# Kernel optimization log

Hardware: AMD Instinct MI355X
Metric: run time of the kernel (lower is better)

## Reference

```python
import jax, jax.numpy as jnp
import numpy as np
from jax.scipy.special import logsumexp


def setup_inputs() -> dict:
    key = jax.random.key(0)
    k = jax.random.split(key, 8)
    B, T, K, L = 32, 128, 16, 16
    s = 0.05
    y_batch = jax.random.uniform(k[0], (B, T, 1, 28, 28), dtype=jnp.float32)
    enc_w1 = jax.random.normal(k[1], (400, 784), dtype=jnp.float32) * s
    enc_b1 = jnp.zeros((400,), jnp.float32)
    enc_w2 = jax.random.normal(k[2], (2 * L, 400), dtype=jnp.float32) * s
    enc_b2 = jnp.zeros((2 * L,), jnp.float32)
    dec_fc_w = jax.random.normal(k[3], (400, L + K), dtype=jnp.float32) * s
    dec_fc_b = jnp.zeros((400,), jnp.float32)
    dec_w = jax.random.normal(k[4], (784, 400), dtype=jnp.float32) * s
    dec_b = jnp.zeros((784,), jnp.float32)
    log_pi = jnp.zeros((K,), jnp.float32)
    log_A = jax.random.normal(k[5], (K, K), dtype=jnp.float32)
    log_A = log_A.at[jnp.arange(K), jnp.arange(K)].set(-1e9)  # fill_diagonal_(-1e9)
    eps = jax.random.normal(k[6], (B * T, L), dtype=jnp.float32)
    return dict(y_batch=y_batch, enc_w1=enc_w1, enc_b1=enc_b1, enc_w2=enc_w2,
                enc_b2=enc_b2, dec_fc_w=dec_fc_w, dec_fc_b=dec_fc_b, dec_w=dec_w,
                dec_b=dec_b, log_pi=log_pi, log_A=log_A, eps=eps)


def reference(y_batch, enc_w1, enc_b1, enc_w2, enc_b2, dec_fc_w, dec_fc_b,
              dec_w, dec_b, log_pi, log_A, eps):
    B, T = y_batch.shape[0], y_batch.shape[1]
    K = log_pi.shape[0]
    L = eps.shape[1]
    N = B * T
    # ---- VAE emission log-likelihoods (compute_log_bk); dropout in eval mode ----
    y_flat = y_batch.reshape(N, 784)
    h = jax.nn.relu(y_flat @ enc_w1.T + enc_b1)                 # [N,400]
    ml = h @ enc_w2.T + enc_b2                                   # [N,2L]
    mu, logvar = ml[:, :L], ml[:, L:]
    z = mu + eps * jnp.exp(0.5 * logvar)                         # reparameterize
    # decode(z, one_hot(k)) for all k at once: split cat-linear into z part + k column
    Wz, Wx = dec_fc_w[:, :L], dec_fc_w[:, L:]                    # [400,L],[400,K]
    base = z @ Wz.T + dec_fc_b                                   # [N,400]
    hk = jax.nn.relu(base[None, :, :] + Wx.T[:, None, :])        # [K,N,400]
    y_rec = jax.nn.sigmoid(jnp.einsum('knh,oh->kno', hk, dec_w) + dec_b)  # [K,N,784]
    # binary_cross_entropy with torch's log clamp at -100
    logp = jnp.clip(jnp.log(y_rec), -100.0, None)
    log1mp = jnp.clip(jnp.log(1.0 - y_rec), -100.0, None)
    bce = -(y_flat[None] * logp + (1.0 - y_flat[None]) * log1mp)  # [K,N,784]
    recon = bce.sum(-1) / 100.0                                   # [K,N]
    log_bk = (-recon).reshape(K, B, T).transpose(1, 2, 0)         # [B,T,K]
    # ---- forward-backward in log domain ----
    lp = jnp.log(jax.nn.softmax(log_pi) + 1e-9)
    lA = jnp.log(jax.nn.softmax(log_A, axis=1) + 1e-9)
    lb_rest = jnp.moveaxis(log_bk[:, 1:], 1, 0)                   # [T-1,B,K]
    a0 = lp + log_bk[:, 0]                                        # [B,K]

    def fstep(prev, lb_t):
        cur = logsumexp(prev[:, :, None] + lA[None], axis=1) + lb_t
        return cur, cur

    _, alphas = jax.lax.scan(fstep, a0, lb_rest)
    log_alpha = jnp.concatenate([a0[:, None], jnp.moveaxis(alphas, 0, 1)], axis=1)  # [B,T,K]

    bT = jnp.zeros((B, K), log_bk.dtype)

    def bstep(nxt, lb_t1):
        cur = logsumexp(lA[None] + (lb_t1 + nxt)[:, None, :], axis=2)
        return cur, cur

    _, betas = jax.lax.scan(bstep, bT, lb_rest, reverse=True)     # betas[t] = beta_t, t=0..T-2
    log_beta = jnp.concatenate([jnp.moveaxis(betas, 0, 1), bT[:, None]], axis=1)  # [B,T,K]

    lg = log_alpha + log_beta
    log_gamma = lg - logsumexp(lg, axis=2, keepdims=True)

    lxi = (log_alpha[:, :-1, :, None] + lA[None, None]
           + (log_bk[:, 1:] + log_beta[:, 1:])[:, :, None, :])    # [B,T-1,K,K]
    lxi = lxi - logsumexp(lxi, axis=(2, 3), keepdims=True)
    return jnp.exp(log_gamma), jnp.exp(lxi)
```

## Files before the change

kernel.cpp:

```cpp
#include <hip/hip_runtime.h>
#include <math.h>


typedef _Float16 h8v __attribute__((ext_vector_type(8)));
typedef _Float16 h4v __attribute__((ext_vector_type(4)));
typedef float f16v __attribute__((ext_vector_type(16)));

__global__ __launch_bounds__(256)
void k_prep(const float* __restrict__ dw, const float* __restrict__ ew1,
            _Float16* __restrict__ dwh, _Float16* __restrict__ w1h,
            float* __restrict__ lb) {
  int idx = blockIdx.x * 256 + threadIdx.x;
  if (idx < 65536) lb[idx] = 0.f;
  if (idx < 896 * 448) {
    int o = idx / 448, h2 = idx - o * 448;
    float v = (o < 784 && h2 < 400) ? dw[o * 400 + h2] : 0.f;
    dwh[idx] = (_Float16)v;
  } else if (idx < 896 * 448 + 512 * 800) {
    int j = idx - 896 * 448;
    int i = j / 800, kc = j - i * 800;
    float v = (i < 400 && kc < 784) ? ew1[i * 784 + kc] : 0.f;
    w1h[j] = (_Float16)v;
  }
}

#define E1ST 40
__global__ __launch_bounds__(256, 2)
void k_enc1(const float* __restrict__ y, const _Float16* __restrict__ w1h,
            const float* __restrict__ b1, float* __restrict__ hout) {
  __shared__ __align__(16) _Float16 Ah[64 * E1ST];
  __shared__ __align__(16) _Float16 Bh[128 * E1ST];
  const int tid = threadIdx.x;
  const int i0 = blockIdx.x * 128;
  const int n0 = blockIdx.y * 64;
  const int wav = tid >> 6, lane = tid & 63;
  const int wn = wav >> 1, wi = wav & 1;
  const int ln = lane & 31, kg = lane >> 5;

  f16v acc[2];
#pragma unroll
  for (int j = 0; j < 2; ++j)
#pragma unroll
    for (int r = 0; r < 16; ++r) acc[j][r] = 0.f;

  const int ar = tid >> 3, ac4 = (tid & 7) * 4;
  const int br = tid >> 2, bg = (tid & 3) * 8;

#pragma unroll 1
  for (int hc = 0; hc < 25; ++hc) {
    const int h0 = hc * 32;
    __syncthreads();
#pragma unroll
    for (int it = 0; it < 2; ++it) {
      int r = ar + 32 * it;
      float4 a = make_float4(0.f, 0.f, 0.f, 0.f);
      if (h0 + ac4 < 784) a = *(const float4*)&y[(n0 + r) * 784 + h0 + ac4];
      h4v hv;
      hv[0] = (_Float16)a.x; hv[1] = (_Float16)a.y;
      hv[2] = (_Float16)a.z; hv[3] = (_Float16)a.w;
      *(h4v*)&Ah[r * E1ST + ac4] = hv;
    }
#pragma unroll
    for (int it = 0; it < 2; ++it) {
      int r = br + 64 * it;
      *(h8v*)&Bh[r * E1ST + bg] = *(const h8v*)&w1h[(i0 + r) * 800 + h0 + bg];
    }
    __syncthreads();
#pragma unroll
    for (int kk = 0; kk < 2; ++kk) {
      const int ko = kk * 16 + kg * 8;
      h8v a  = *(const h8v*)&Ah[(wn * 32 + ln) * E1ST + ko];
      h8v b0 = *(const h8v*)&Bh[(wi * 64 + ln) * E1ST + ko];
      h8v b1 = *(const h8v*)&Bh[(wi * 64 + 32 + ln) * E1ST + ko];
      acc[0] = __builtin_amdgcn_mfma_f32_32x32x16_f16(a, b0, acc[0], 0, 0, 0);
      acc[1] = __builtin_amdgcn_mfma_f32_32x32x16_f16(a, b1, acc[1], 0, 0, 0);
    }
  }
#pragma unroll
  for (int j = 0; j < 2; ++j) {
    const int i = i0 + wi * 64 + j * 32 + ln;
    if (i < 400) {
      const float bias = b1[i];
#pragma unroll
      for (int reg = 0; reg < 16; ++reg) {
        const int row = n0 + wn * 32 + (reg & 3) + 8 * (reg >> 2) + 4 * kg;
        hout[row * 400 + i] = fmaxf(acc[j][reg] + bias, 0.f);
      }
    }
  }
}

__global__ __launch_bounds__(128, 4)
void k_enc2z(const float* __restrict__ h, const float* __restrict__ w2,
             const float* __restrict__ b2, const float* __restrict__ eps,
             float* __restrict__ z) {
  __shared__ __align__(16) float h_lds[4 * 400];
  __shared__ __align__(16) float w2_lds[32 * 404];
  __shared__ float ml_lds[4 * 32];
  const int tid = threadIdx.x;
  const int n0 = blockIdx.x * 4;
  for (int idx = tid; idx < 400; idx += 128) {
    int r = idx / 100, c = idx % 100;
    *(float4*)&h_lds[r * 400 + c * 4] = *(const float4*)&h[(n0 + r) * 400 + c * 4];
  }
  for (int idx = tid; idx < 3200; idx += 128) {
    int r = idx / 100, c = idx % 100;
    *(float4*)&w2_lds[r * 404 + c * 4] = *(const float4*)&w2[r * 400 + c * 4];
  }
  __syncthreads();
  const int c_ = tid & 31, n_ = tid >> 5;
  float acc = 0.f;
  for (int q = 0; q < 100; ++q) {
    float4 hv = *(const float4*)&h_lds[n_ * 400 + q * 4];
    float4 wv = *(const float4*)&w2_lds[c_ * 404 + q * 4];
    acc += hv.x * wv.x + hv.y * wv.y + hv.z * wv.z + hv.w * wv.w;
  }
  ml_lds[n_ * 32 + c_] = acc + b2[c_];
  __syncthreads();
  if (tid < 64) {
    int n2 = tid >> 4, l = tid & 15;
    float mu = ml_lds[n2 * 32 + l];
    float lv = ml_lds[n2 * 32 + 16 + l];
    z[(n0 + n2) * 16 + l] = mu + eps[(n0 + n2) * 16 + l] * expf(0.5f * lv);
  }
}

__global__ __launch_bounds__(256, 4)
void k_base(const float* __restrict__ z, const float* __restrict__ dfw,
            const float* __restrict__ dfb, float* __restrict__ basep) {
  __shared__ float z_lds[16 * 16];
  __shared__ __align__(16) float wz_lds[400 * 20];
  const int tid = threadIdx.x;
  const int n0 = blockIdx.x * 16;
  if (tid < 64) {
    int n = tid >> 2, c = (tid & 3) * 4;
    *(float4*)&z_lds[n * 16 + c] = *(const float4*)&z[(n0 + n) * 16 + c];
  }
  for (int idx = tid; idx < 1600; idx += 256) {
    int i = idx >> 2, c = (idx & 3) * 4;
    *(float4*)&wz_lds[i * 20 + c] = *(const float4*)&dfw[i * 32 + c];
  }
  __syncthreads();
  for (int idx = tid; idx < 7168; idx += 256) {
    int n = idx / 448, i = idx - n * 448;
    float acc = 0.f;
    if (i < 400) {
      acc = dfb[i];
#pragma unroll
      for (int q = 0; q < 4; ++q) {
        float4 zv = *(const float4*)&z_lds[n * 16 + q * 4];
        float4 wv = *(const float4*)&wz_lds[i * 20 + q * 4];
        acc += zv.x * wv.x + zv.y * wv.y + zv.z * wv.z + zv.w * wv.w;
      }
    }
    basep[(n0 + n) * 448 + i] = acc;
  }
}

#define DST 72
__global__ __launch_bounds__(256, 2)
void k_dec(const float* __restrict__ basep, const float* __restrict__ dfw,
           const _Float16* __restrict__ dwh, const float* __restrict__ decb,
           const float* __restrict__ y, float* __restrict__ lb) {
  __shared__ __align__(16) _Float16 Ah[128 * DST];
  __shared__ __align__(16) _Float16 Bh[128 * DST];
  __shared__ float wx[448];
  __shared__ float red[256];

  const int tid = threadIdx.x;
  const int id  = blockIdx.x;
  const int lin = (id & 7) * 448 + (id >> 3);
  const int n_i = lin / 112;
  const int rem = lin - n_i * 112;
  const int k   = rem / 7;
  const int ot  = rem - k * 7;
  const int n0  = n_i * 128;
  const int o0  = ot * 128;
  const bool full = (ot < 6);

  const int wav = tid >> 6, lane = tid & 63;
  const int wn = wav >> 1, wo = wav & 1;
  const int ln = lane & 31, kg = lane >> 5;

  for (int i = tid; i < 448; i += 256) wx[i] = (i < 400) ? dfw[i * 32 + 16 + k] : 0.f;

  const int ar = tid >> 4, ac4 = (tid & 15) * 4;
  const int br = tid >> 3, bg = (tid & 7) * 8;
  const float* aptr = basep + (long)(n0 + ar) * 448 + ac4;

  float4 apf[8];
#pragma unroll
  for (int it = 0; it < 8; ++it) apf[it] = *(const float4*)&aptr[(16 * it) * 448];

  f16v acc[2][2];
#pragma unroll
  for (int i = 0; i < 2; ++i)
#pragma unroll
    for (int j = 0; j < 2; ++j)
#pragma unroll
      for (int r = 0; r < 16; ++r) acc[i][j][r] = 0.f;

#pragma unroll 1
  for (int hc = 0; hc < 7; ++hc) {
    const int h0 = hc * 64;
    h8v bpf[4];
#pragma unroll
    for (int it = 0; it < 4; ++it)
      bpf[it] = *(const h8v*)&dwh[(o0 + br + 32 * it) * 448 + h0 + bg];
    __syncthreads();
    {
      float4 w = *(const float4*)&wx[h0 + ac4];
#pragma unroll
      for (int it = 0; it < 8; ++it) {
        int r = ar + 16 * it;
        h4v hv;
        hv[0] = (_Float16)fmaxf(apf[it].x + w.x, 0.f);
        hv[1] = (_Float16)fmaxf(apf[it].y + w.y, 0.f);
        hv[2] = (_Float16)fmaxf(apf[it].z + w.z, 0.f);
        hv[3] = (_Float16)fmaxf(apf[it].w + w.w, 0.f);
        *(h4v*)&Ah[r * DST + ac4] = hv;
      }
    }
#pragma unroll
    for (int it = 0; it < 4; ++it)
      *(h8v*)&Bh[(br + 32 * it) * DST + bg] = bpf[it];
    __syncthreads();
    if (hc < 6) {
      const int hn = (hc + 1) * 64;
#pragma unroll
      for (int it = 0; it < 8; ++it)
        apf[it] = *(const float4*)&aptr[(16 * it) * 448 + hn];
    }
#pragma unroll
    for (int kk = 0; kk < 4; ++kk) {
      const int ko = kk * 16 + kg * 8;
      h8v a0 = *(const h8v*)&Ah[(wn * 64 + ln) * DST + ko];
      h8v a1 = *(const h8v*)&Ah[(wn * 64 + 32 + ln) * DST + ko];
      h8v b0 = *(const h8v*)&Bh[(wo * 64 + ln) * DST + ko];
      h8v b1 = *(const h8v*)&Bh[(wo * 64 + 32 + ln) * DST + ko];
      if (full) {
        acc[0][0] = __builtin_amdgcn_mfma_f32_32x32x16_f16(a0, b0, acc[0][0], 0, 0, 0);
        acc[1][0] = __builtin_amdgcn_mfma_f32_32x32x16_f16(a1, b0, acc[1][0], 0, 0, 0);
        acc[0][1] = __builtin_amdgcn_mfma_f32_32x32x16_f16(a0, b1, acc[0][1], 0, 0, 0);
        acc[1][1] = __builtin_amdgcn_mfma_f32_32x32x16_f16(a1, b1, acc[1][1], 0, 0, 0);
      } else if (wo == 0) {
        acc[0][0] = __builtin_amdgcn_mfma_f32_32x32x16_f16(a0, b0, acc[0][0], 0, 0, 0);
        acc[1][0] = __builtin_amdgcn_mfma_f32_32x32x16_f16(a1, b0, acc[1][0], 0, 0, 0);
      }
    }
  }
  const int obase = o0 + wo * 64;
  const float bj0 = (obase + ln < 784) ? decb[obase + ln] : 0.f;
  const float bj1 = (obase + 32 + ln < 784) ? decb[obase + 32 + ln] : 0.f;
#pragma unroll
  for (int i = 0; i < 2; ++i) {
#pragma unroll
    for (int reg = 0; reg < 16; ++reg) {
      const int row = wn * 64 + i * 32 + (reg & 3) + 8 * (reg >> 2) + 4 * kg;
      float v = 0.f;
#pragma unroll
      for (int j = 0; j < 2; ++j) {
        const int o = obase + j * 32 + ln;
        if (o < 784) {
          float x = acc[i][j][reg] + (j ? bj1 : bj0);
          float yv = y[(n0 + row) * 784 + o];
          float spx = fmaxf(x, 0.f) + __logf(1.f + __expf(-fabsf(x)));
          float t2 = fminf(spx, 100.f);
          float t1 = fminf(spx - x, 100.f);
          v += t2 + yv * (t1 - t2);
        }
      }
      v += __shfl_xor(v, 1, 64);
      v += __shfl_xor(v, 2, 64);
      v += __shfl_xor(v, 4, 64);
      v += __shfl_xor(v, 8, 64);
      v += __shfl_xor(v, 16, 64);
      if (ln == 0) red[wo * 128 + row] = v;
    }
  }
  __syncthreads();
  if (tid < 128) {
    float s = red[tid] + red[128 + tid];
    atomicAdd(&lb[(n0 + tid) * 16 + k], s);
  }
}

__global__ __launch_bounds__(256, 2)
void k_hmm(const float* __restrict__ lb, const float* __restrict__ lpi,
           const float* __restrict__ lA, float* __restrict__ out,
           float* __restrict__ g_ah, float* __restrict__ g_pb,
           float* __restrict__ g_sinv, float* __restrict__ g_Al) {
  __shared__ float btl[128 * 16];
  __shared__ float ah[128 * 16];
  __shared__ float bh[128 * 16];
  __shared__ float braw[128 * 16];
  __shared__ float A_l[16 * 17];
  __shared__ float pi_l[16];
  const int tid = threadIdx.x;
  const int b = blockIdx.x;

  for (int idx = tid; idx < 512; idx += 256) {
    float4 v = *(const float4*)&lb[b * 2048 + idx * 4];
    v.x *= -0.01f; v.y *= -0.01f; v.z *= -0.01f; v.w *= -0.01f;
    *(float4*)&btl[idx * 4] = v;
  }
  if (tid < 16) {
    const int j = tid;
    float m = -1e30f;
#pragma unroll
    for (int q = 0; q < 16; ++q) m = fmaxf(m, lA[j * 16 + q]);
    float e[16]; float s = 0.f;
#pragma unroll
    for (int q = 0; q < 16; ++q) { e[q] = expf(lA[j * 16 + q] - m); s += e[q]; }
    float inv = 1.f / s;
#pragma unroll
    for (int q = 0; q < 16; ++q) {
      float v = e[q] * inv + 1e-9f;
      A_l[j * 17 + q] = v;
      g_Al[j * 16 + q] = v;
    }
  } else if (tid == 16) {
    float m = -1e30f;
#pragma unroll
    for (int q = 0; q < 16; ++q) m = fmaxf(m, lpi[q]);
    float e[16]; float s = 0.f;
#pragma unroll
    for (int q = 0; q < 16; ++q) { e[q] = expf(lpi[q] - m); s += e[q]; }
    float inv = 1.f / s;
#pragma unroll
    for (int q = 0; q < 16; ++q) pi_l[q] = e[q] * inv + 1e-9f;
  }
  __syncthreads();
  if (tid < 128) {
    const int t = tid;
    float v[16]; float m = -1e30f;
#pragma unroll
    for (int q = 0; q < 16; ++q) { v[q] = btl[t * 16 + q]; m = fmaxf(m, v[q]); }
#pragma unroll
    for (int q = 0; q < 16; ++q) btl[t * 16 + q] = expf(v[q] - m);
  }
  __syncthreads();
  const int lane = tid & 63;
  const int kk = lane & 15, grp = lane >> 4;
  if (tid < 64) {
    float v0 = pi_l[kk] * btl[kk];
    float ss0 = v0;
    ss0 += __shfl_xor(ss0, 1, 64); ss0 += __shfl_xor(ss0, 2, 64);
    ss0 += __shfl_xor(ss0, 4, 64); ss0 += __shfl_xor(ss0, 8, 64);
    if (grp == 0) ah[kk] = v0 / ss0;
    for (int t = 1; t < 128; ++t) {
      float acc = 0.f;
#pragma unroll
      for (int jj = 0; jj < 4; ++jj) {
        int j = grp * 4 + jj;
        acc = fmaf(ah[(t - 1) * 16 + j], A_l[j * 17 + kk], acc);
      }
      acc += __shfl_xor(acc, 16, 64);
      acc += __shfl_xor(acc, 32, 64);
      float v = acc * btl[t * 16 + kk];
      float ss = v;
      ss += __shfl_xor(ss, 1, 64); ss += __shfl_xor(ss, 2, 64);
      ss += __shfl_xor(ss, 4, 64); ss += __shfl_xor(ss, 8, 64);
      if (grp == 0) ah[t * 16 + kk] = v / ss;
    }
  } else if (tid < 128) {
    if (grp == 0) bh[127 * 16 + kk] = 1.f;
    for (int t = 126; t >= 0; --t) {
      float acc = 0.f;
#pragma unroll
      for (int q = 0; q < 4; ++q) {
        int k2 = grp * 4 + q;
        acc = fmaf(A_l[kk * 17 + k2], btl[(t + 1) * 16 + k2] * bh[(t + 1) * 16 + k2], acc);
      }
      acc += __shfl_xor(acc, 16, 64);
      acc += __shfl_xor(acc, 32, 64);
      float ss = acc;
      ss += __shfl_xor(ss, 1, 64); ss += __shfl_xor(ss, 2, 64);
      ss += __shfl_xor(ss, 4, 64); ss += __shfl_xor(ss, 8, 64);
      if (grp == 0) { braw[t * 16 + kk] = acc; bh[t * 16 + kk] = acc / ss; }
    }
  }
  __syncthreads();
  if (tid < 128) {
    const int t = tid;
    float g[16]; float s2 = 0.f;
#pragma unroll
    for (int q = 0; q < 16; ++q) { g[q] = ah[t * 16 + q] * bh[t * 16 + q]; s2 += g[q]; }
    float inv = 1.f / s2;
#pragma unroll
    for (int c = 0; c < 4; ++c) {
      float4 o;
      o.x = g[c * 4 + 0] * inv; o.y = g[c * 4 + 1] * inv;
      o.z = g[c * 4 + 2] * inv; o.w = g[c * 4 + 3] * inv;
      *(float4*)&out[(b * 128 + t) * 16 + c * 4] = o;
      float4 av = *(float4*)&ah[t * 16 + c * 4];
      *(float4*)&g_ah[(b * 128 + t) * 16 + c * 4] = av;
      float4 p;
      p.x = btl[t * 16 + c * 4 + 0] * bh[t * 16 + c * 4 + 0];
      p.y = btl[t * 16 + c * 4 + 1] * bh[t * 16 + c * 4 + 1];
      p.z = btl[t * 16 + c * 4 + 2] * bh[t * 16 + c * 4 + 2];
      p.w = btl[t * 16 + c * 4 + 3] * bh[t * 16 + c * 4 + 3];
      *(float4*)&g_pb[(b * 128 + t) * 16 + c * 4] = p;
    }
  } else {
    const int t = tid - 128;
    if (t < 127) {
      float s2 = 0.f;
#pragma unroll
      for (int q = 0; q < 16; ++q) s2 += ah[t * 16 + q] * braw[t * 16 + q];
      g_sinv[b * 128 + t] = 1.f / s2;
    }
  }
}

__global__ __launch_bounds__(256)
void k_xi(const float* __restrict__ g_ah, const float* __restrict__ g_pb,
          const float* __restrict__ g_sinv, const float* __restrict__ g_Al,
          float* __restrict__ out) {
  const int b = blockIdx.x, t = blockIdx.y;
  const int tid = threadIdx.x;
  const int j = tid >> 4, k2 = tid & 15;
  float val = g_ah[(b * 128 + t) * 16 + j] * g_Al[j * 16 + k2] *
              g_pb[(b * 128 + t + 1) * 16 + k2] * g_sinv[b * 128 + t];
  out[65536 + (b * 127 + t) * 256 + tid] = val;
}

extern "C" void kernel_launch(void* const* d_in, const int* in_sizes, int n_in,
                              void* d_out, int out_size, void* d_ws, size_t ws_size,
                              hipStream_t stream) {
  (void)in_sizes; (void)n_in; (void)out_size; (void)ws_size;
  const float* y   = (const float*)d_in[0];
  const float* ew1 = (const float*)d_in[1];
  const float* eb1 = (const float*)d_in[2];
  const float* ew2 = (const float*)d_in[3];
  const float* eb2 = (const float*)d_in[4];
  const float* dfw = (const float*)d_in[5];
  const float* dfb = (const float*)d_in[6];
  const float* dw  = (const float*)d_in[7];
  const float* db  = (const float*)d_in[8];
  const float* lpi = (const float*)d_in[9];
  const float* lA  = (const float*)d_in[10];
  const float* eps = (const float*)d_in[11];
  float* out = (float*)d_out;

  float* ws = (float*)d_ws;
  float* h      = ws;
  float* basep  = ws;
  float* z      = ws + 1835008;
  float* lb     = z + 65536;
  _Float16* dwh = (_Float16*)(lb + 65536);
  _Float16* w1h = dwh + 896 * 448;
  float* g_ah   = (float*)(w1h + 512 * 800);
  float* g_pb   = g_ah + 65536;
  float* g_sinv = g_pb + 65536;
  float* g_Al   = g_sinv + 4096;

  k_prep<<<3168, 256, 0, stream>>>(dw, ew1, dwh, w1h, lb);
  k_enc1<<<dim3(4, 64), 256, 0, stream>>>(y, w1h, eb1, h);
  k_enc2z<<<1024, 128, 0, stream>>>(h, ew2, eb2, eps, z);
  k_base<<<256, 256, 0, stream>>>(z, dfw, dfb, basep);
  k_dec<<<3584, 256, 0, stream>>>(basep, dfw, dwh, db, y, lb);
  k_hmm<<<32, 256, 0, stream>>>(lb, lpi, lA, out, g_ah, g_pb, g_sinv, g_Al);
  k_xi<<<dim3(32, 127), 256, 0, stream>>>(g_ah, g_pb, g_sinv, g_Al, out);
}
```

Baseline: 347.6 us.

## Precompute fp16 hidden activations per state and stream into decoder via global_load_lds

Adds a kernel that builds relu(base + Wx[k]) for all 16 states as an fp16 tensor in workspace. A new decoder GEMM then loads A and B tiles straight into LDS with global_load_lds, using XOR swizzling instead of padded rows. This removes the per-tile in-kernel construction and conversion of hidden activations, at the cost of writing and re-reading a roughly 59 MB fp16 buffer. The new path only runs when the workspace is large enough. Separately, the encoder second layer now handles 16 rows per block with 4 accumulators per thread, so each W2 load is reused four times.

```diff
diff --git a/kernel.cpp b/kernel.cpp
--- a/kernel.cpp
+++ b/kernel.cpp
@@ -5,6 +5,12 @@
 typedef _Float16 h8v __attribute__((ext_vector_type(8)));
 typedef _Float16 h4v __attribute__((ext_vector_type(4)));
 typedef float f16v __attribute__((ext_vector_type(16)));
+
+__device__ __forceinline__ void gll16(const void* g, void* l) {
+  __builtin_amdgcn_global_load_lds(
+      (const __attribute__((address_space(1))) void*)g,
+      (__attribute__((address_space(3))) void*)l, 16, 0, 0);
+}
 
 __global__ __launch_bounds__(256)
 void k_prep(const float* __restrict__ dw, const float* __restrict__ ew1,
@@ -90,35 +96,45 @@
   }
 }
 
-__global__ __launch_bounds__(128, 4)
+__global__ __launch_bounds__(128, 2)
 void k_enc2z(const float* __restrict__ h, const float* __restrict__ w2,
              const float* __restrict__ b2, const float* __restrict__ eps,
              float* __restrict__ z) {
-  __shared__ __align__(16) float h_lds[4 * 400];
+  __shared__ __align__(16) float h_lds[16 * 400];
   __shared__ __align__(16) float w2_lds[32 * 404];
-  __shared__ float ml_lds[4 * 32];
-  const int tid = threadIdx.x;
-  const int n0 = blockIdx.x * 4;
-  for (int idx = tid; idx < 400; idx += 128) {
-    int r = idx / 100, c = idx % 100;
+  __shared__ float ml_lds[16 * 32];
+  const int tid = threadIdx.x;
+  const int n0 = blockIdx.x * 16;
+  for (int idx = tid; idx < 1600; idx += 128) {
+    int r = idx / 100, c = idx - r * 100;
     *(float4*)&h_lds[r * 400 + c * 4] = *(const float4*)&h[(n0 + r) * 400 + c * 4];
   }
   for (int idx = tid; idx < 3200; idx += 128) {
-    int r = idx / 100, c = idx % 100;
+    int r = idx / 100, c = idx - r * 100;
     *(float4*)&w2_lds[r * 404 + c * 4] = *(const float4*)&w2[r * 400 + c * 4];
   }
   __syncthreads();
-  const int c_ = tid & 31, n_ = tid >> 5;
-  float acc = 0.f;
+  const int c_ = tid & 31, n4 = tid >> 5;
+  float a0 = 0.f, a1 = 0.f, a2 = 0.f, a3 = 0.f;
   for (int q = 0; q < 100; ++q) {
-    float4 hv = *(const float4*)&h_lds[n_ * 400 + q * 4];
     float4 wv = *(const float4*)&w2_lds[c_ * 404 + q * 4];
-    acc += hv.x * wv.x + hv.y * wv.y + hv.z * wv.z + hv.w * wv.w;
-  }
-  ml_lds[n_ * 32 + c_] = acc + b2[c_];
-  __syncthreads();
-  if (tid < 64) {
-    int n2 = tid >> 4, l = tid & 15;
+    float4 h0 = *(const float4*)&h_lds[(n4 * 4 + 0) * 400 + q * 4];
+    float4 h1 = *(const float4*)&h_lds[(n4 * 4 + 1) * 400 + q * 4];
+    float4 h2 = *(const float4*)&h_lds[(n4 * 4 + 2) * 400 + q * 4];
+    float4 h3 = *(const float4*)&h_lds[(n4 * 4 + 3) * 400 + q * 4];
+    a0 += h0.x * wv.x + h0.y * wv.y + h0.z * wv.z + h0.w * wv.w;
+    a1 += h1.x * wv.x + h1.y * wv.y + h1.z * wv.z + h1.w * wv.w;
+    a2 += h2.x * wv.x + h2.y * wv.y + h2.z * wv.z + h2.w * wv.w;
+    a3 += h3.x * wv.x + h3.y * wv.y + h3.z * wv.z + h3.w * wv.w;
+  }
+  const float bb = b2[c_];
+  ml_lds[(n4 * 4 + 0) * 32 + c_] = a0 + bb;
+  ml_lds[(n4 * 4 + 1) * 32 + c_] = a1 + bb;
+  ml_lds[(n4 * 4 + 2) * 32 + c_] = a2 + bb;
+  ml_lds[(n4 * 4 + 3) * 32 + c_] = a3 + bb;
+  __syncthreads();
+  for (int t = tid; t < 256; t += 128) {
+    int n2 = t >> 4, l = t & 15;
     float mu = ml_lds[n2 * 32 + l];
     float lv = ml_lds[n2 * 32 + 16 + l];
     z[(n0 + n2) * 16 + l] = mu + eps[(n0 + n2) * 16 + l] * expf(0.5f * lv);
@@ -157,11 +173,152 @@
   }
 }
 
+__global__ __launch_bounds__(256, 4)
+void k_hk(const float* __restrict__ basep, const float* __restrict__ dfw,
+          _Float16* __restrict__ hkh) {
+  __shared__ float wxT[16 * 448];
+  const int tid = threadIdx.x;
+  const int n0 = blockIdx.x * 8;
+  for (int idx = tid; idx < 7168; idx += 256) {
+    int k = idx / 448, hh = idx - k * 448;
+    wxT[idx] = (hh < 400) ? dfw[hh * 32 + 16 + k] : 0.f;
+  }
+  __syncthreads();
+  for (int s = tid; s < 448; s += 256) {
+    int r = s / 56, c8 = s - r * 56;
+    const float* bp = &basep[(size_t)(n0 + r) * 448 + c8 * 8];
+    float4 b0 = *(const float4*)bp;
+    float4 b1 = *(const float4*)(bp + 4);
+#pragma unroll
+    for (int k = 0; k < 16; ++k) {
+      const float* wp = &wxT[k * 448 + c8 * 8];
+      float4 w0 = *(const float4*)wp;
+      float4 w1 = *(const float4*)(wp + 4);
+      h8v o;
+      o[0] = (_Float16)fmaxf(b0.x + w0.x, 0.f);
+      o[1] = (_Float16)fmaxf(b0.y + w0.y, 0.f);
+      o[2] = (_Float16)fmaxf(b0.z + w0.z, 0.f);
+      o[3] = (_Float16)fmaxf(b0.w + w0.w, 0.f);
+      o[4] = (_Float16)fmaxf(b1.x + w1.x, 0.f);
+      o[5] = (_Float16)fmaxf(b1.y + w1.y, 0.f);
+      o[6] = (_Float16)fmaxf(b1.z + w1.z, 0.f);
+      o[7] = (_Float16)fmaxf(b1.w + w1.w, 0.f);
+      *(h8v*)&hkh[((size_t)k * 4096 + n0 + r) * 448 + c8 * 8] = o;
+    }
+  }
+}
+
+__global__ __launch_bounds__(256, 2)
+void k_dec2(const _Float16* __restrict__ hkh, const _Float16* __restrict__ dwh,
+            const float* __restrict__ decb, const float* __restrict__ y,
+            float* __restrict__ lb) {
+  __shared__ __align__(16) _Float16 Ah[128 * 64];
+  __shared__ __align__(16) _Float16 Bh[128 * 64];
+  __shared__ float red[256];
+
+  const int tid = threadIdx.x;
+  const int id  = blockIdx.x;
+  const int lin = (id & 7) * 448 + (id >> 3);
+  const int n_i = lin / 112;
+  const int rem = lin - n_i * 112;
+  const int k   = rem / 7;
+  const int ot  = rem - k * 7;
+  const int n0  = n_i * 128;
+  const int o0  = ot * 128;
+
+  const int wav = tid >> 6, lane = tid & 63;
+  const int wn = wav >> 1, wo = wav & 1;
+  const int ln = lane & 31, kg = lane >> 5;
+
+  const int l8 = lane >> 3, l7 = lane & 7;
+  const int swh = (l7 * 8) ^ (l8 * 8);
+  const _Float16* hkk = hkh + (size_t)k * 4096 * 448;
+  const _Float16* pA[4];
+  const _Float16* pB[4];
+#pragma unroll
+  for (int i = 0; i < 4; ++i) {
+    const int row = wav * 32 + i * 8 + l8;
+    pA[i] = hkk + (size_t)(n0 + row) * 448 + swh;
+    pB[i] = dwh + (size_t)(o0 + row) * 448 + swh;
+  }
+
+  f16v acc[2][2];
+#pragma unroll
+  for (int i = 0; i < 2; ++i)
+#pragma unroll
+    for (int j = 0; j < 2; ++j)
+#pragma unroll
+      for (int r = 0; r < 16; ++r) acc[i][j][r] = 0.f;
+
+  const int sx = (ln & 7) * 8;
+  const int e0 = (kg * 8) ^ sx;
+  const int arow = (wn * 64 + ln) * 64;
+  const int brow = (wo * 64 + ln) * 64;
+
+#pragma unroll 1
+  for (int hc = 0; hc < 7; ++hc) {
+    __syncthreads();
+#pragma unroll
+    for (int i = 0; i < 4; ++i) {
+      gll16(pA[i], &Ah[(wav * 4 + i) * 512]);
+      gll16(pB[i], &Bh[(wav * 4 + i) * 512]);
+      pA[i] += 64; pB[i] += 64;
+    }
+    __syncthreads();
+#pragma unroll
+    for (int kk = 0; kk < 4; ++kk) {
+      const int cx = (kk * 16) ^ e0;
+      h8v a0 = *(const h8v*)&Ah[arow + cx];
+      h8v a1 = *(const h8v*)&Ah[arow + 2048 + cx];
+      h8v b0 = *(const h8v*)&Bh[brow + cx];
+      h8v b1 = *(const h8v*)&Bh[brow + 2048 + cx];
+      acc[0][0] = __builtin_amdgcn_mfma_f32_32x32x16_f16(a0, b0, acc[0][0], 0, 0, 0);
+      acc[1][0] = __builtin_amdgcn_mfma_f32_32x32x16_f16(a1, b0, acc[1][0], 0, 0, 0);
+      acc[0][1] = __builtin_amdgcn_mfma_f32_32x32x16_f16(a0, b1, acc[0][1], 0, 0, 0);
+      acc[1][1] = __builtin_amdgcn_mfma_f32_32x32x16_f16(a1, b1, acc[1][1], 0, 0, 0);
+    }
+  }
+  const int obase = o0 + wo * 64;
+  const float bj0 = (obase + ln < 784) ? decb[obase + ln] : 0.f;
+  const float bj1 = (obase + 32 + ln < 784) ? decb[obase + 32 + ln] : 0.f;
+#pragma unroll
+  for (int i = 0; i < 2; ++i) {
+#pragma unroll
+    for (int reg = 0; reg < 16; ++reg) {
+      const int row = wn * 64 + i * 32 + (reg & 3) + 8 * (reg >> 2) + 4 * kg;
+      float v = 0.f;
+#pragma unroll
+      for (int j = 0; j < 2; ++j) {
+        const int o = obase + j * 32 + ln;
+        if (o < 784) {
+          float x = acc[i][j][reg] + (j ? bj1 : bj0);
+          float yv = y[(n0 + row) * 784 + o];
+          float spx = fmaxf(x, 0.f) + __logf(1.f + __expf(-fabsf(x)));
+          float t2 = fminf(spx, 100.f);
+          float t1 = fminf(spx - x, 100.f);
+          v += t2 + yv * (t1 - t2);
+        }
+      }
+      v += __shfl_xor(v, 1, 64);
+      v += __shfl_xor(v, 2, 64);
+      v += __shfl_xor(v, 4, 64);
+      v += __shfl_xor(v, 8, 64);
+      v += __shfl_xor(v, 16, 64);
+      if (ln == 0) red[wo * 128 + row] = v;
+    }
+  }
+  __syncthreads();
+  if (tid < 128) {
+    float s = red[tid] + red[128 + tid];
+    atomicAdd(&lb[(n0 + tid) * 16 + k], s);
+  }
+}
+
 #define DST 72
 __global__ __launch_bounds__(256, 2)
-void k_dec(const float* __restrict__ basep, const float* __restrict__ dfw,
-           const _Float16* __restrict__ dwh, const float* __restrict__ decb,
-           const float* __restrict__ y, float* __restrict__ lb) {
+void k_dec1(const float* __restrict__ basep, const float* __restrict__ dfw,
+            const _Float16* __restrict__ dwh, const float* __restrict__ decb,
+            const float* __restrict__ y, float* __restrict__ lb) {
   __shared__ __align__(16) _Float16 Ah[128 * DST];
   __shared__ __align__(16) _Float16 Bh[128 * DST];
   __shared__ float wx[448];
@@ -428,7 +585,7 @@
 extern "C" void kernel_launch(void* const* d_in, const int* in_sizes, int n_in,
                               void* d_out, int out_size, void* d_ws, size_t ws_size,
                               hipStream_t stream) {
-  (void)in_sizes; (void)n_in; (void)out_size; (void)ws_size;
+  (void)in_sizes; (void)n_in; (void)out_size;
   const float* y   = (const float*)d_in[0];
   const float* ew1 = (const float*)d_in[1];
   const float* eb1 = (const float*)d_in[2];
@@ -454,12 +611,20 @@
   float* g_pb   = g_ah + 65536;
   float* g_sinv = g_pb + 65536;
   float* g_Al   = g_sinv + 4096;
+  _Float16* hkh = (_Float16*)(g_Al + 256);
+
+  const bool big_ws = (ws_size >= 68748288ull);
 
   k_prep<<<3168, 256, 0, stream>>>(dw, ew1, dwh, w1h, lb);
   k_enc1<<<dim3(4, 64), 256, 0, stream>>>(y, w1h, eb1, h);
-  k_enc2z<<<1024, 128, 0, stream>>>(h, ew2, eb2, eps, z);
+  k_enc2z<<<256, 128, 0, stream>>>(h, ew2, eb2, eps, z);
   k_base<<<256, 256, 0, stream>>>(z, dfw, dfb, basep);
-  k_dec<<<3584, 256, 0, stream>>>(basep, dfw, dwh, db, y, lb);
+  if (big_ws) {
+    k_hk<<<512, 256, 0, stream>>>(basep, dfw, hkh);
+    k_dec2<<<3584, 256, 0, stream>>>(hkh, dwh, db, y, lb);
+  } else {
+    k_dec1<<<3584, 256, 0, stream>>>(basep, dfw, dwh, db, y, lb);
+  }
   k_hmm<<<32, 256, 0, stream>>>(lb, lpi, lA, out, g_ah, g_pb, g_sinv, g_Al);
   k_xi<<<dim3(32, 127), 256, 0, stream>>>(g_ah, g_pb, g_sinv, g_Al, out);
 }
```

Result: faster. 335.5 us (-3.5%).
